# Performance work log

Measured on AMD Instinct MI355X. Metric: run time of the kernel, lower is better.

The kernel has to match this reference:

```python
import jax, jax.numpy as jnp
import numpy as np

L, B, H = 4096, 32, 512


def setup_inputs() -> dict:
    key = jax.random.key(0)
    k1, k2, k3, k4 = jax.random.split(key, 4)
    query = jax.random.normal(k1, (B, H), dtype=jnp.float32)
    key_val = jax.random.normal(k2, (L, B, H), dtype=jnp.float32)
    # torch Linear(2H, H, bias=False): weight is (H, 2H); we store transposed (2H, H)
    W = jax.random.normal(k3, (2 * H, H), dtype=jnp.float32) * (1.0 / np.sqrt(2 * H))
    v = jax.random.normal(k4, (H,), dtype=jnp.float32)
    return {"query": query, "key_val": key_val, "W": W, "v": v}


def reference(query, key_val, W, v):
    # concat([expand(query), key], -1) @ W == query @ W_q + key @ W_k
    Wq, Wk = W[:H], W[H:]                       # each (H, H)
    q_proj = query @ Wq                          # (B, H)
    k_proj = jnp.einsum('lbi,ih->lbh', key_val, Wk)  # (L, B, H)
    energy = jnp.tanh(q_proj[None, :, :] + k_proj)   # (L, B, H)
    scores = jnp.einsum('h,lbh->bl', v, energy)      # (B, L)
    return jax.nn.softmax(scores, axis=1)[:, None, :]  # (B, 1, L)
```

## Files before the change

### kernel.cpp

```cpp
#include <hip/hip_runtime.h>
#include <hip/hip_bf16.h>
#include <stdint.h>

#define L_DIM 4096
#define B_DIM 32
#define H_DIM 512
#define M_DIM (L_DIM * B_DIM)
#define K_DIM H_DIM

typedef _Float16 half8 __attribute__((ext_vector_type(8)));
typedef __fp16 fp16x2 __attribute__((ext_vector_type(2)));
typedef float floatx4 __attribute__((ext_vector_type(4)));

__device__ __forceinline__ float tanh_fast(float x) {
  float e = __builtin_amdgcn_exp2f(x * 2.88539008177793f);
  return 1.0f - 2.0f * __builtin_amdgcn_rcpf(e + 1.0f);
}

__device__ __forceinline__ uint2 pack4(const float4& f) {
  const fp16x2 p0 = __builtin_amdgcn_cvt_pkrtz(f.x, f.y);
  const fp16x2 p1 = __builtin_amdgcn_cvt_pkrtz(f.z, f.w);
  uint2 u;
  u.x = __builtin_bit_cast(unsigned, p0);
  u.y = __builtin_bit_cast(unsigned, p1);
  return u;
}

__device__ __forceinline__ void gload_lds16(const float* g, float* l) {
  __builtin_amdgcn_global_load_lds(
      (__attribute__((address_space(1))) void*)g,
      (__attribute__((address_space(3))) void*)l, 16, 0, 0);
}

#define VM_WAIT(n) asm volatile("s_waitcnt vmcnt(" #n ")" ::: "memory")

__global__ __launch_bounds__(512) void prep_kernel(const float* __restrict__ query,
                                                   const float* __restrict__ W,
                                                   float* __restrict__ qp,
                                                   _Float16* __restrict__ W2) {
  __shared__ float4 qred[512];
  if (blockIdx.x < 64) {
    const int t = blockIdx.x * 512 + threadIdx.x;
    const int l15 = t & 15;
    const int q = (t >> 4) & 3;
    const int nc = (t >> 6) & 31;
    const int kt = t >> 11;
    const int n = nc * 16 + l15;
    const int kbase = H_DIM + kt * 32 + q * 8;
    half8 h;
#pragma unroll
    for (int j = 0; j < 8; ++j)
      h[j] = (_Float16)W[(size_t)(kbase + j) * H_DIM + n];
    *(half8*)(W2 + (size_t)t * 8) = h;
  } else {
    const int b = blockIdx.x - 64;
    const int tid = threadIdx.x;
    const int hx = tid & 127;
    const int ky = tid >> 7;
    const int h = hx * 4;
    const float* qrow = query + b * H_DIM + ky * 128;
    const float* wrow = W + (size_t)(ky * 128) * H_DIM + h;
    float4 acc = make_float4(0.f, 0.f, 0.f, 0.f);
#pragma unroll 8
    for (int i = 0; i < 128; ++i) {
      const float qv = qrow[i];
      const float4 w4 = *(const float4*)(wrow + (size_t)i * H_DIM);
      acc.x += qv * w4.x; acc.y += qv * w4.y;
      acc.z += qv * w4.z; acc.w += qv * w4.w;
    }
    qred[tid] = acc;
    __syncthreads();
    if (ky == 0) {
      const float4 a1 = qred[tid + 128], a2 = qred[tid + 256], a3 = qred[tid + 384];
      acc.x += a1.x + a2.x + a3.x;
      acc.y += a1.y + a2.y + a3.y;
      acc.z += a1.z + a2.z + a3.z;
      acc.w += a1.w + a2.w + a3.w;
      *(float4*)(qp + (size_t)b * H_DIM + h) = acc;
    }
  }
}

__global__ __launch_bounds__(512, 4) void fused_gemm_kernel(
    const float* __restrict__ key, const _Float16* __restrict__ W2,
    const float* __restrict__ qp, const float* __restrict__ v,
    float* __restrict__ scores) {
  __shared__ __align__(16) float As[4][64 * 32];
  __shared__ float swave[8 * 64];

  const int tid = threadIdx.x;
  const int lane = tid & 63;
  const int wn = tid >> 6;
  const int l15 = lane & 15;
  const int quad = lane >> 4;
  const int m0 = blockIdx.x * 64;

  const int srow = tid >> 3;
  const int lc = (tid & 7) ^ (srow & 7);
  const float* ag = key + (size_t)(m0 + srow) * K_DIM + lc * 4;
  float* lbase = &As[0][0] + wn * 256;

  const half8* bptr = (const half8*)W2 + (size_t)(wn * 4) * 64 + lane;

  floatx4 acc[4][4];
#pragma unroll
  for (int fm = 0; fm < 4; ++fm)
#pragma unroll
    for (int fn = 0; fn < 4; ++fn) acc[fm][fn] = (floatx4)0.0f;

  half8 bn[2][4];

  gload_lds16(ag, lbase);
  gload_lds16(ag + 32, lbase + 2048);
  gload_lds16(ag + 64, lbase + 4096);
#pragma unroll
  for (int fn = 0; fn < 4; ++fn) bn[0][fn] = bptr[fn * 64];
  bptr += 32 * 64;

#pragma unroll
  for (int kt = 0; kt < 16; ++kt) {
    if (kt == 0)       VM_WAIT(6);
    else if (kt == 1)  VM_WAIT(10);
    else if (kt == 14) VM_WAIT(13);
    else if (kt == 15) VM_WAIT(12);
    else               VM_WAIT(14);
    __builtin_amdgcn_sched_barrier(0);
    __builtin_amdgcn_s_barrier();
    __builtin_amdgcn_sched_barrier(0);

    if (kt < 13) {
      gload_lds16(ag + (kt + 3) * 32, lbase + ((kt + 3) & 3) * 2048);
    }
    if (kt < 15) {
#pragma unroll
      for (int fn = 0; fn < 4; ++fn) bn[(kt + 1) & 1][fn] = bptr[fn * 64];
      bptr += 32 * 64;
    }

    const float* buf = &As[kt & 3][0];
    half8 av[4];
#pragma unroll
    for (int fm = 0; fm < 4; ++fm) {
      const int rbase = (fm * 16 + l15) * 32;
      const float4 f0 = *(const float4*)(buf + rbase + (((2 * quad + 0) ^ (l15 & 7)) * 4));
      const float4 f1 = *(const float4*)(buf + rbase + (((2 * quad + 1) ^ (l15 & 7)) * 4));
      const uint2 u0 = pack4(f0);
      const uint2 u1 = pack4(f1);
      const uint4 uu = make_uint4(u0.x, u0.y, u1.x, u1.y);
      av[fm] = __builtin_bit_cast(half8, uu);
    }
#pragma unroll
    for (int fm = 0; fm < 4; ++fm)
#pragma unroll
      for (int fn = 0; fn < 4; ++fn)
        acc[fm][fn] = __builtin_amdgcn_mfma_f32_16x16x32_f16(av[fm], bn[kt & 1][fn],
                                                             acc[fm][fn], 0, 0, 0);
  }

  float vv[4];
#pragma unroll
  for (int fn = 0; fn < 4; ++fn) vv[fn] = v[wn * 64 + fn * 16 + l15];

#pragma unroll
  for (int fm = 0; fm < 4; ++fm) {
#pragma unroll
    for (int r = 0; r < 4; ++r) {
      const int mrow = fm * 16 + quad * 4 + r;
      const float* qrow = qp + (size_t)(mrow & 31) * H_DIM;
      float rs = 0.f;
#pragma unroll
      for (int fn = 0; fn < 4; ++fn) {
        const int n = wn * 64 + fn * 16 + l15;
        const float x = qrow[n] + acc[fm][fn][r];
        rs += vv[fn] * tanh_fast(x);
      }
      rs += __shfl_xor(rs, 1);
      rs += __shfl_xor(rs, 2);
      rs += __shfl_xor(rs, 4);
      rs += __shfl_xor(rs, 8);
      if (l15 == 0) swave[wn * 64 + mrow] = rs;
    }
  }
  __syncthreads();
  if (tid < 64) {
    float s = 0.f;
#pragma unroll
    for (int j = 0; j < 8; ++j) s += swave[j * 64 + tid];
    const int m = m0 + tid;
    scores[(size_t)(m & 31) * L_DIM + (m >> 5)] = s;
  }
}

__global__ __launch_bounds__(256) void softmax_kernel(const float* __restrict__ scores,
                                                      float* __restrict__ out) {
  const int b = blockIdx.x;
  const int t = threadIdx.x;
  const int lane = t & 63;
  const int w = t >> 6;
  __shared__ float redm[4], reds[4];
  const float* srow = scores + (size_t)b * L_DIM;
  float s[16];
#pragma unroll
  for (int i = 0; i < 16; ++i) s[i] = srow[t + i * 256];
  float mx = s[0];
#pragma unroll
  for (int i = 1; i < 16; ++i) mx = fmaxf(mx, s[i]);
#pragma unroll
  for (int off = 1; off < 64; off <<= 1) mx = fmaxf(mx, __shfl_xor(mx, off));
  if (lane == 0) redm[w] = mx;
  __syncthreads();
  mx = fmaxf(fmaxf(redm[0], redm[1]), fmaxf(redm[2], redm[3]));
  float sum = 0.f;
#pragma unroll
  for (int i = 0; i < 16; ++i) {
    s[i] = __builtin_amdgcn_exp2f((s[i] - mx) * 1.44269504f);
    sum += s[i];
  }
#pragma unroll
  for (int off = 1; off < 64; off <<= 1) sum += __shfl_xor(sum, off);
  if (lane == 0) reds[w] = sum;
  __syncthreads();
  const float inv = 1.0f / (reds[0] + reds[1] + reds[2] + reds[3]);
#pragma unroll
  for (int i = 0; i < 16; ++i) out[(size_t)b * L_DIM + t + i * 256] = s[i] * inv;
}

extern "C" void kernel_launch(void* const* d_in, const int* in_sizes, int n_in,
                              void* d_out, int out_size, void* d_ws, size_t ws_size,
                              hipStream_t stream) {
  const float* query = (const float*)d_in[0];
  const float* key   = (const float*)d_in[1];
  const float* W     = (const float*)d_in[2];
  const float* v     = (const float*)d_in[3];
  float* out = (float*)d_out;

  char* ws = (char*)d_ws;
  float* qp       = (float*)ws;
  float* scores   = (float*)(ws + 65536);
  _Float16* W2    = (_Float16*)(ws + 65536 + 524288);

  prep_kernel<<<96, 512, 0, stream>>>(query, W, qp, W2);
  fused_gemm_kernel<<<M_DIM / 64, 512, 0, stream>>>(key, W2, qp, v, scores);
  softmax_kernel<<<B_DIM, 256, 0, stream>>>(scores, out);
}
```

Before: 428.8 us.

## Convert key tiles to fp16 once on load into double-buffered LDS

Replaces the direct global-to-LDS fp32 loads, which used a 4-stage buffer, with register-staged global loads. Each thread converts its key chunk to fp16 once and writes it into a 2-stage fp16 LDS buffer, so each element is converted by one thread instead of by every wave that reads it. LDS footprint and read bandwidth halve, and the swizzled fp32 reads become plain half8 reads. The cost is a shallower prefetch, a register round-trip for the key loads, W2 fragments loaded inside the loop without prefetch, and possible bank conflicts on the unswizzled fp16 layout.

```diff
diff --git a/kernel.cpp b/kernel.cpp
--- a/kernel.cpp
+++ b/kernel.cpp
@@ -25,14 +25,6 @@
   u.y = __builtin_bit_cast(unsigned, p1);
   return u;
 }
-
-__device__ __forceinline__ void gload_lds16(const float* g, float* l) {
-  __builtin_amdgcn_global_load_lds(
-      (__attribute__((address_space(1))) void*)g,
-      (__attribute__((address_space(3))) void*)l, 16, 0, 0);
-}
-
-#define VM_WAIT(n) asm volatile("s_waitcnt vmcnt(" #n ")" ::: "memory")
 
 __global__ __launch_bounds__(512) void prep_kernel(const float* __restrict__ query,
                                                    const float* __restrict__ W,
@@ -85,7 +77,7 @@
     const float* __restrict__ key, const _Float16* __restrict__ W2,
     const float* __restrict__ qp, const float* __restrict__ v,
     float* __restrict__ scores) {
-  __shared__ __align__(16) float As[4][64 * 32];
+  __shared__ __align__(16) _Float16 As[2][64 * 32];
   __shared__ float swave[8 * 64];
 
   const int tid = threadIdx.x;
@@ -96,9 +88,9 @@
   const int m0 = blockIdx.x * 64;
 
   const int srow = tid >> 3;
-  const int lc = (tid & 7) ^ (srow & 7);
-  const float* ag = key + (size_t)(m0 + srow) * K_DIM + lc * 4;
-  float* lbase = &As[0][0] + wn * 256;
+  const int schunk = tid & 7;
+  const float* ag = key + (size_t)(m0 + srow) * K_DIM + schunk * 4;
+  const int adst = srow * 32 + schunk * 4;
 
   const half8* bptr = (const half8*)W2 + (size_t)(wn * 4) * 64 + lane;
 
@@ -108,53 +100,44 @@
 #pragma unroll
     for (int fn = 0; fn < 4; ++fn) acc[fm][fn] = (floatx4)0.0f;
 
-  half8 bn[2][4];
-
-  gload_lds16(ag, lbase);
-  gload_lds16(ag + 32, lbase + 2048);
-  gload_lds16(ag + 64, lbase + 4096);
-#pragma unroll
-  for (int fn = 0; fn < 4; ++fn) bn[0][fn] = bptr[fn * 64];
-  bptr += 32 * 64;
+  float4 ra0 = *(const float4*)(ag);
+  float4 rb[2];
+  rb[1] = *(const float4*)(ag + 32);
+  rb[0] = *(const float4*)(ag + 64);
+  *(uint2*)(As[0] + adst) = pack4(ra0);
+  asm volatile("s_waitcnt lgkmcnt(0)" ::: "memory");
+  __builtin_amdgcn_s_barrier();
+  __builtin_amdgcn_sched_barrier(0);
 
 #pragma unroll
   for (int kt = 0; kt < 16; ++kt) {
-    if (kt == 0)       VM_WAIT(6);
-    else if (kt == 1)  VM_WAIT(10);
-    else if (kt == 14) VM_WAIT(13);
-    else if (kt == 15) VM_WAIT(12);
-    else               VM_WAIT(14);
+    half8 bc[4];
+#pragma unroll
+    for (int fn = 0; fn < 4; ++fn) bc[fn] = bptr[fn * 64];
+    bptr += 32 * 64;
+
+    const _Float16* buf = As[kt & 1];
+    half8 av[4];
+#pragma unroll
+    for (int fm = 0; fm < 4; ++fm)
+      av[fm] = *(const half8*)(buf + (fm * 16 + l15) * 32 + quad * 8);
+
+    if (kt < 15) {
+      *(uint2*)(As[(kt + 1) & 1] + adst) = pack4(rb[(kt + 1) & 1]);
+      if (kt < 13) rb[(kt + 1) & 1] = *(const float4*)(ag + (kt + 3) * 32);
+    }
+
+#pragma unroll
+    for (int fm = 0; fm < 4; ++fm)
+#pragma unroll
+      for (int fn = 0; fn < 4; ++fn)
+        acc[fm][fn] = __builtin_amdgcn_mfma_f32_16x16x32_f16(av[fm], bc[fn],
+                                                             acc[fm][fn], 0, 0, 0);
+
     __builtin_amdgcn_sched_barrier(0);
+    asm volatile("s_waitcnt lgkmcnt(0)" ::: "memory");
     __builtin_amdgcn_s_barrier();
     __builtin_amdgcn_sched_barrier(0);
-
-    if (kt < 13) {
-      gload_lds16(ag + (kt + 3) * 32, lbase + ((kt + 3) & 3) * 2048);
-    }
-    if (kt < 15) {
-#pragma unroll
-      for (int fn = 0; fn < 4; ++fn) bn[(kt + 1) & 1][fn] = bptr[fn * 64];
-      bptr += 32 * 64;
-    }
-
-    const float* buf = &As[kt & 3][0];
-    half8 av[4];
-#pragma unroll
-    for (int fm = 0; fm < 4; ++fm) {
-      const int rbase = (fm * 16 + l15) * 32;
-      const float4 f0 = *(const float4*)(buf + rbase + (((2 * quad + 0) ^ (l15 & 7)) * 4));
-      const float4 f1 = *(const float4*)(buf + rbase + (((2 * quad + 1) ^ (l15 & 7)) * 4));
-      const uint2 u0 = pack4(f0);
-      const uint2 u1 = pack4(f1);
-      const uint4 uu = make_uint4(u0.x, u0.y, u1.x, u1.y);
-      av[fm] = __builtin_bit_cast(half8, uu);
-    }
-#pragma unroll
-    for (int fm = 0; fm < 4; ++fm)
-#pragma unroll
-      for (int fn = 0; fn < 4; ++fn)
-        acc[fm][fn] = __builtin_amdgcn_mfma_f32_16x16x32_f16(av[fm], bn[kt & 1][fn],
-                                                             acc[fm][fn], 0, 0, 0);
   }
 
   float vv[4];
```

Result: no change. 422.2 us (-1.5%).
